# Kernel tuning notes

Hardware: AMD Instinct MI355X
Metric: run time of the kernel (lower is better)

## Reference

```python
import jax, jax.numpy as jnp
import numpy as np

BL = 5           # block_len
BS = BL * BL     # block_size = 25
NH = 8           # num_heads
MASK_ONES = 12   # first 12 window positions unmasked (causal raster mask)


def _rel_pos_index():
    coords = np.stack(np.meshgrid(np.arange(BL), np.arange(BL), indexing='ij')).reshape(2, -1)
    rel = coords[:, :, None] - coords[:, None, :]          # [2, 25, 25]
    idx = (rel[0] + BL - 1) * (2 * BL - 1) + (rel[1] + BL - 1)
    return idx                                              # [25, 25] int

_REL_IDX = _rel_pos_index()


def _layernorm(x, w, b, eps=1e-5):
    m = jnp.mean(x, axis=-1, keepdims=True)
    v = jnp.var(x, axis=-1, keepdims=True)
    return (x - m) * jax.lax.rsqrt(v + eps) * w + b


def setup_inputs() -> dict:
    key = jax.random.key(0)
    ks = jax.random.split(key, 16)
    B, C, H, W = 4, 64, 64, 64
    out_dim = 64
    hidden = int(C * 4.0)
    s = lambda k, shape, scale=0.02: jax.random.normal(k, shape, dtype=jnp.float32) * scale
    return {
        'x': jax.random.normal(ks[0], (B, C, H, W), dtype=jnp.float32),
        'norm1_w': jnp.ones((C,), jnp.float32), 'norm1_b': jnp.zeros((C,), jnp.float32),
        'qkv_w': s(ks[1], (3 * C, C)), 'qkv_b': s(ks[2], (3 * C,)),
        'rpb_table': s(ks[3], ((2 * BL - 1) * (2 * BL - 1), NH)),
        'norm2_w': jnp.ones((C,), jnp.float32), 'norm2_b': jnp.zeros((C,), jnp.float32),
        'fc1_w': s(ks[4], (hidden, C)), 'fc1_b': s(ks[5], (hidden,)),
        'fc2_w': s(ks[6], (C, hidden)), 'fc2_b': s(ks[7], (C,)),
        'proj_w': s(ks[8], (out_dim, C)), 'proj_b': s(ks[9], (out_dim,)),
    }


def reference(x, norm1_w, norm1_b, qkv_w, qkv_b, rpb_table,
              norm2_w, norm2_b, fc1_w, fc1_b, fc2_w, fc2_b, proj_w, proj_b):
    B, C, H, W = x.shape
    hd = C // NH
    scale = hd ** (-0.5)

    # F.unfold(kernel=5, pad=2): per-pixel 5x5 neighborhood, channel-major then (kh,kw)
    xp = jnp.pad(x, ((0, 0), (0, 0), (2, 2), (2, 2)))
    patches = jnp.stack([xp[:, :, i:i + H, j:j + W] for i in range(BL) for j in range(BL)], axis=2)  # [B,C,25,H,W]
    x_unfold = patches.reshape(B, C, BS, H * W).transpose(0, 3, 2, 1)  # [B,HW,25,C]

    mask = (jnp.arange(BS) < MASK_ONES).astype(x.dtype)[None, None, :, None]
    x_masked = x_unfold * mask

    out = _layernorm(x_masked, norm1_w, norm1_b)
    qkv = out @ qkv_w.T + qkv_b                                 # [B,HW,25,3C]
    qkv = qkv.reshape(B, H * W, BS, 3, NH, hd).transpose(3, 0, 1, 4, 2, 5)  # [3,B,HW,nh,25,hd]
    q, k, v = qkv[0] * scale, qkv[1], qkv[2]

    attn = jnp.einsum('bpnqd,bpnkd->bpnqk', q, k)               # [B,HW,nh,25,25]
    bias = rpb_table[_REL_IDX.reshape(-1)].reshape(BS, BS, NH).transpose(2, 0, 1)  # [nh,25,25]
    attn = jax.nn.softmax(attn + bias[None, None], axis=-1)

    o = jnp.einsum('bpnqk,bpnkd->bpnqd', attn, v)               # [B,HW,nh,25,hd]
    o = o.transpose(0, 1, 3, 2, 4).reshape(B, H * W, BS, C)
    o = o + x_masked
    out_sumed = jnp.sum(o, axis=2)                              # [B,HW,C]

    y = _layernorm(out_sumed, norm2_w, norm2_b)
    y = jax.nn.gelu(y @ fc1_w.T + fc1_b, approximate=False) @ fc2_w.T + fc2_b
    y = y + out_sumed
    y = y @ proj_w.T + proj_b                                   # [B,HW,out_dim]
    return y.reshape(B, H, W, -1).transpose(0, 3, 1, 2)
```

## Files before the change

### kernel.cpp

```cpp
#include <hip/hip_runtime.h>
#include <hip/hip_bf16.h>


typedef _Float16 h2f __attribute__((ext_vector_type(2)));

__device__ __forceinline__ float fdot2f(h2f a, h2f b, float c) {
#if defined(__has_builtin)
#if __has_builtin(__builtin_amdgcn_fdot2)
    return __builtin_amdgcn_fdot2(a, b, c, false);
#else
    return c + (float)a.x * (float)b.x + (float)a.y * (float)b.y;
#endif
#else
    return c + (float)a.x * (float)b.x + (float)a.y * (float)b.y;
#endif
}

__device__ __forceinline__ float frcp(float x) {
#if defined(__has_builtin)
#if __has_builtin(__builtin_amdgcn_rcpf)
    return __builtin_amdgcn_rcpf(x);
#else
    return 1.0f / x;
#endif
#else
    return 1.0f / x;
#endif
}

#define SC 0.35355339059327373f

__global__ __launch_bounds__(256) void k_qkv(
    const float* __restrict__ x, const float* __restrict__ n1w, const float* __restrict__ n1b,
    const float* __restrict__ qw, const float* __restrict__ qb, const float* __restrict__ rpb,
    float* __restrict__ qkv_all, float* __restrict__ qkvc,
    float* __restrict__ eb, float* __restrict__ ebs)
{
    const int t = threadIdx.x;
    if (blockIdx.x == 256) {
        if (t < 192) {
            float acc = qb[t];
            for (int c = 0; c < 64; ++c) acc += n1b[c] * qw[t * 64 + c];
            qkvc[t] = acc;
        }
        for (int i = t; i < 2400; i += 256) {
            int h = i / 300, r = i % 300, q = r / 12, k = r % 12;
            int idx = (q / 5 - k / 5 + 4) * 9 + (q % 5 - k % 5 + 4);
            eb[i] = __expf(rpb[idx * 8 + h]);
        }
        for (int i = t; i < 200; i += 256) {
            int h = i / 25, q = i % 25;
            float s = 0.f;
            for (int k = 12; k < 25; ++k) {
                int idx = (q / 5 - k / 5 + 4) * 9 + (q % 5 - k % 5 + 4);
                s += __expf(rpb[idx * 8 + h]);
            }
            ebs[i] = s;
        }
        return;
    }
    __shared__ float sw[12288];
    for (int i = t * 4; i < 12288; i += 1024)
        *(float4*)(sw + i) = *(const float4*)(qw + i);
    __syncthreads();
    const int lane = t & 63, g = t >> 6;
    const int p = blockIdx.x * 64 + lane;
    const int b = p >> 12, hw = p & 4095;
    const float* xp = x + b * 262144 + hw;
    float xr[64];
    float s = 0.f;
#pragma unroll
    for (int c = 0; c < 64; ++c) { float v = xp[c * 4096]; xr[c] = v; s += v; }
    float m = s * 0.015625f;
    float s2 = 0.f;
#pragma unroll
    for (int c = 0; c < 64; ++c) { float d = xr[c] - m; s2 += d * d; }
    float rstd = rsqrtf(s2 * 0.015625f + 1e-5f);
#pragma unroll
    for (int c = 0; c < 64; ++c) xr[c] = (xr[c] - m) * rstd * n1w[c] + n1b[c];
    float* orow = qkv_all + (size_t)p * 192;
    for (int i = 0; i < 48; ++i) {
        int o = g * 48 + i;
        const float* wr = sw + o * 64;
        float acc = qb[o];
#pragma unroll
        for (int c = 0; c < 64; ++c) acc += xr[c] * wr[c];
        orow[o] = acc;
    }
}

__global__ __launch_bounds__(256) void k_attn(
    const float* __restrict__ x, const float* __restrict__ qkv_all,
    const float* __restrict__ qkvc, const float* __restrict__ eb, const float* __restrict__ ebs,
    float* __restrict__ osT)
{
    __shared__ float sq[108 * 194];
    __shared__ float sx[108 * 66];
    __shared__ float seb[2400];
    __shared__ float sebs[200];
    __shared__ float sqc[192];
    const int t = threadIdx.x;
    const int p0 = blockIdx.x * 32;
    const int b = p0 >> 12;
    const int hw0 = p0 & 4095;
    const int hrow = hw0 >> 6, w0 = hw0 & 63;

    for (int i = t; i < 192; i += 256) sqc[i] = qkvc[i];
    for (int i = t; i < 2400; i += 256) seb[i] = eb[i];
    for (int i = t; i < 200; i += 256) sebs[i] = ebs[i];
    for (int idx = t; idx < 108 * 96; idx += 256) {
        int row = idx / 96, o2 = (idx - row * 96) * 2;
        int rr = row / 36, cc = row - rr * 36;
        int gr = hrow - 2 + rr, gc = w0 - 2 + cc;
        float2 v;
        if (gr >= 0 && gc >= 0 && gc < 64)
            v = *(const float2*)(qkv_all + (size_t)((b << 12) + (gr << 6) + gc) * 192 + o2);
        else
            v = make_float2(qkvc[o2], qkvc[o2 + 1]);
        *(float2*)(sq + row * 194 + o2) = v;
    }
    for (int idx = t; idx < 6912; idx += 256) {
        int r = idx / 2304, rem = idx - r * 2304, c = rem / 36, ww = rem - c * 36;
        int gr = hrow - 2 + r, gc = w0 - 2 + ww;
        float v = (gr >= 0 && gc >= 0 && gc < 64) ? x[b * 262144 + c * 4096 + (gr << 6) + gc] : 0.f;
        sx[(r * 36 + ww) * 66 + c] = v;
    }
    __syncthreads();

    const int pix = t & 31, h = t >> 5, hb = h * 8;

    float xs[8];
#pragma unroll
    for (int d = 0; d < 8; ++d) xs[d] = 0.f;
#pragma unroll
    for (int s = 0; s < 12; ++s) {
        const float* xr = sx + ((s / 5) * 36 + pix + (s % 5)) * 66 + hb;
#pragma unroll
        for (int d = 0; d < 8; ++d) xs[d] += xr[d];
    }
    float qch[8];
#pragma unroll
    for (int d = 0; d < 8; ++d) qch[d] = sqc[hb + d] * SC;
    float edc[12], ecc;
#pragma unroll
    for (int k = 0; k < 13; ++k) {
        const float* kp = (k < 12) ? (sq + ((k / 5) * 36 + pix + (k % 5)) * 194 + 64 + hb)
                                   : (sqc + 64 + hb);
        float dd = 0.f;
#pragma unroll
        for (int d = 0; d < 8; ++d) dd += qch[d] * kp[d];
        if (k < 12) edc[k] = __expf(dd); else ecc = __expf(dd);
    }
    float w[12], wc = 0.f;
#pragma unroll
    for (int k = 0; k < 12; ++k) w[k] = 0.f;

#pragma unroll
    for (int qc = 0; qc < 3; ++qc) {
        float qr[4][8];
#pragma unroll
        for (int qq = 0; qq < 4; ++qq) {
            const int s = qc * 4 + qq;
            const float* qp = sq + ((s / 5) * 36 + pix + (s % 5)) * 194 + hb;
#pragma unroll
            for (int d = 0; d < 8; ++d) qr[qq][d] = qp[d] * SC;
        }
        float er[4][13];
#pragma unroll
        for (int k = 0; k < 13; ++k) {
            float kr[8];
            const float* kp = (k < 12) ? (sq + ((k / 5) * 36 + pix + (k % 5)) * 194 + 64 + hb)
                                       : (sqc + 64 + hb);
#pragma unroll
            for (int d = 0; d < 8; ++d) kr[d] = kp[d];
#pragma unroll
            for (int qq = 0; qq < 4; ++qq) {
                float dd = 0.f;
#pragma unroll
                for (int d = 0; d < 8; ++d) dd += qr[qq][d] * kr[d];
                er[qq][k] = dd;
            }
        }
#pragma unroll
        for (int qq = 0; qq < 4; ++qq) {
            const int s = qc * 4 + qq;
            const float* ebr = seb + (h * 25 + s) * 12;
            float ebsv = sebs[h * 25 + s];
            float ec = __expf(er[qq][12]);
            float tt[12];
            float rs = ec * ebsv;
#pragma unroll
            for (int k = 0; k < 12; ++k) { float e = __expf(er[qq][k]) * ebr[k]; tt[k] = e; rs += e; }
            float inv = frcp(rs);
#pragma unroll
            for (int k = 0; k < 12; ++k) w[k] += tt[k] * inv;
            wc += ec * ebsv * inv;
        }
    }
#pragma unroll
    for (int q = 12; q < 25; ++q) {
        const float* ebr = seb + (h * 25 + q) * 12;
        float ebsv = sebs[h * 25 + q];
        float rs = ecc * ebsv;
        float tt[12];
#pragma unroll
        for (int k = 0; k < 12; ++k) { float e = edc[k] * ebr[k]; tt[k] = e; rs += e; }
        float inv = frcp(rs);
#pragma unroll
        for (int k = 0; k < 12; ++k) w[k] += tt[k] * inv;
        wc += ecc * ebsv * inv;
    }
    float out[8];
#pragma unroll
    for (int d = 0; d < 8; ++d) out[d] = wc * sqc[128 + hb + d];
#pragma unroll
    for (int k = 0; k < 12; ++k) {
        const float* vr = sq + ((k / 5) * 36 + pix + (k % 5)) * 194 + 128 + hb;
#pragma unroll
        for (int d = 0; d < 8; ++d) out[d] += w[k] * vr[d];
    }
    const int p = p0 + pix;
#pragma unroll
    for (int d = 0; d < 8; ++d) osT[(size_t)(hb + d) * 16384 + p] = out[d] + xs[d];
}

__global__ __launch_bounds__(512) void k_mlp(
    const float* __restrict__ osT, const float* __restrict__ n2w, const float* __restrict__ n2b,
    const float* __restrict__ w1, const float* __restrict__ b1,
    const float* __restrict__ w2, const float* __restrict__ b2,
    const float* __restrict__ pw, const float* __restrict__ pb,
    float* __restrict__ out)
{
    __shared__ _Float16 sW1[16384];
    __shared__ _Float16 sW2[16384];
    __shared__ float sP[4096];
    __shared__ _Float16 sH[64 * 258];
    __shared__ float sY[64 * 66];
    __shared__ float sb1[256], sb2[64], spb[64];
    const int t = threadIdx.x;
    for (int i = t; i < 16384; i += 512) sW1[i] = (_Float16)w1[i];
    for (int i = t; i < 16384; i += 512) sW2[i] = (_Float16)w2[i];
    for (int i = t; i < 4096; i += 512) sP[i] = pw[i];
    if (t < 256) sb1[t] = b1[t];
    if (t < 64) { sb2[t] = b2[t]; spb[t] = pb[t]; }
    __syncthreads();
    const int pix = t & 63, sl = t >> 6;
    const int p = blockIdx.x * 64 + pix;
    float a[64];
    float s = 0.f;
#pragma unroll
    for (int c = 0; c < 64; ++c) { float v = osT[(size_t)c * 16384 + p]; a[c] = v; s += v; }
    float m = s * 0.015625f;
    float s2 = 0.f;
#pragma unroll
    for (int c = 0; c < 64; ++c) { float d = a[c] - m; s2 += d * d; }
    float rstd = rsqrtf(s2 * 0.015625f + 1e-5f);
    h2f av[32];
#pragma unroll
    for (int c = 0; c < 32; ++c) {
        float e0 = (a[2 * c] - m) * rstd * n2w[2 * c] + n2b[2 * c];
        float e1 = (a[2 * c + 1] - m) * rstd * n2w[2 * c + 1] + n2b[2 * c + 1];
        h2f v; v.x = (_Float16)e0; v.y = (_Float16)e1;
        av[c] = v;
    }
    for (int i = 0; i < 32; ++i) {
        int j = sl * 32 + i;
        const h2f* wr = (const h2f*)(sW1 + j * 64);
        float acc = sb1[j];
#pragma unroll
        for (int cp = 0; cp < 32; ++cp) acc = fdot2f(av[cp], wr[cp], acc);
        float g = 0.5f * acc * (1.f + erff(acc * 0.70710678118654752f));
        sH[pix * 258 + j] = (_Float16)g;
    }
    __syncthreads();
#pragma unroll
    for (int mm = 0; mm < 8; ++mm) {
        int o = sl * 8 + mm;
        const h2f* wr = (const h2f*)(sW2 + o * 256);
        const h2f* hr = (const h2f*)(sH + pix * 258);
        float acc = sb2[o];
#pragma unroll 32
        for (int jp = 0; jp < 128; ++jp) acc = fdot2f(hr[jp], wr[jp], acc);
        float resid = osT[(size_t)o * 16384 + p];
        sY[pix * 66 + o] = acc + resid;
    }
    __syncthreads();
    const int bimg = p >> 12, hw = p & 4095, hh = hw >> 6, ww = hw & 63;
#pragma unroll
    for (int mm = 0; mm < 8; ++mm) {
        int o = sl * 8 + mm;
        const float* wr = sP + o * 64;
        const float* yr = sY + pix * 66;
        float acc = spb[o];
#pragma unroll
        for (int c = 0; c < 64; ++c) acc += yr[c] * wr[c];
        out[(size_t)(((bimg * 64 + o) * 64 + hh) * 64) + ww] = acc;
    }
}

extern "C" void kernel_launch(void* const* d_in, const int* in_sizes, int n_in,
                              void* d_out, int out_size, void* d_ws, size_t ws_size,
                              hipStream_t stream) {
    const float* x   = (const float*)d_in[0];
    const float* n1w = (const float*)d_in[1];
    const float* n1b = (const float*)d_in[2];
    const float* qw  = (const float*)d_in[3];
    const float* qb  = (const float*)d_in[4];
    const float* rpb = (const float*)d_in[5];
    const float* n2w = (const float*)d_in[6];
    const float* n2b = (const float*)d_in[7];
    const float* w1  = (const float*)d_in[8];
    const float* b1  = (const float*)d_in[9];
    const float* w2  = (const float*)d_in[10];
    const float* b2  = (const float*)d_in[11];
    const float* pw  = (const float*)d_in[12];
    const float* pb  = (const float*)d_in[13];
    float* out = (float*)d_out;

    float* ws = (float*)d_ws;
    float* qkv_all = ws;
    float* osT     = qkv_all + 16384 * 192;
    float* qkvc    = osT + 64 * 16384;
    float* eb      = qkvc + 192;
    float* ebs     = eb + 2400;

    hipLaunchKernelGGL(k_qkv, dim3(257), dim3(256), 0, stream,
                       x, n1w, n1b, qw, qb, rpb, qkv_all, qkvc, eb, ebs);
    hipLaunchKernelGGL(k_attn, dim3(512), dim3(256), 0, stream,
                       x, qkv_all, qkvc, eb, ebs, osT);
    hipLaunchKernelGGL(k_mlp, dim3(256), dim3(512), 0, stream,
                       osT, n2w, n2b, w1, b1, w2, b2, pw, pb, out);
}
```

Baseline: 224.0 us.

## Store QKV in fp16, split attention queries across halves, precompute fp16 MLP weights

The QKV projection now uses fp16 dot2 instructions and writes fp16 qkv, which halves the intermediate traffic. The masked x-window residual sum moves into extra blocks of the first kernel, and attention then accumulates into osT. Attention uses 512 threads with the query set split across two halves, reduced through shared memory, and K held in registers as fp16x8. The MLP kernel reads weights that were converted to fp16 once in global memory instead of converting them per block into LDS, and it now uses 32-pixel tiles. These changes lower precision and add a read-modify-write dependency on osT.

```diff
diff --git a/kernel.cpp b/kernel.cpp
--- a/kernel.cpp
+++ b/kernel.cpp
@@ -3,298 +3,329 @@
 
 
 typedef _Float16 h2f __attribute__((ext_vector_type(2)));
+typedef _Float16 h8  __attribute__((ext_vector_type(8)));
+union u8h { h8 v; h2f p[4]; };
 
 __device__ __forceinline__ float fdot2f(h2f a, h2f b, float c) {
 #if defined(__has_builtin)
 #if __has_builtin(__builtin_amdgcn_fdot2)
     return __builtin_amdgcn_fdot2(a, b, c, false);
 #else
-    return c + (float)a.x * (float)b.x + (float)a.y * (float)b.y;
+    return c + (float)a.x*(float)b.x + (float)a.y*(float)b.y;
 #endif
 #else
-    return c + (float)a.x * (float)b.x + (float)a.y * (float)b.y;
+    return c + (float)a.x*(float)b.x + (float)a.y*(float)b.y;
 #endif
 }
-
+__device__ __forceinline__ float dot8(u8h a, u8h b) {
+    float c = 0.f;
+    c = fdot2f(a.p[0], b.p[0], c);
+    c = fdot2f(a.p[1], b.p[1], c);
+    c = fdot2f(a.p[2], b.p[2], c);
+    c = fdot2f(a.p[3], b.p[3], c);
+    return c;
+}
 __device__ __forceinline__ float frcp(float x) {
 #if defined(__has_builtin)
 #if __has_builtin(__builtin_amdgcn_rcpf)
     return __builtin_amdgcn_rcpf(x);
 #else
-    return 1.0f / x;
+    return 1.0f/x;
 #endif
 #else
-    return 1.0f / x;
+    return 1.0f/x;
 #endif
 }
 
 #define SC 0.35355339059327373f
 
-__global__ __launch_bounds__(256) void k_qkv(
+__global__ __launch_bounds__(256, 4) void k_qkv(
     const float* __restrict__ x, const float* __restrict__ n1w, const float* __restrict__ n1b,
     const float* __restrict__ qw, const float* __restrict__ qb, const float* __restrict__ rpb,
-    float* __restrict__ qkv_all, float* __restrict__ qkvc,
-    float* __restrict__ eb, float* __restrict__ ebs)
+    const float* __restrict__ w1, const float* __restrict__ w2, const float* __restrict__ pw,
+    _Float16* __restrict__ qkv, _Float16* __restrict__ qkvc_h,
+    _Float16* __restrict__ ebh, float* __restrict__ ebs,
+    _Float16* __restrict__ w1h, _Float16* __restrict__ w2h, _Float16* __restrict__ pwh,
+    float* __restrict__ osT)
 {
     const int t = threadIdx.x;
-    if (blockIdx.x == 256) {
-        if (t < 192) {
-            float acc = qb[t];
-            for (int c = 0; c < 64; ++c) acc += n1b[c] * qw[t * 64 + c];
-            qkvc[t] = acc;
+    const int bid = blockIdx.x;
+    if (bid >= 512) {
+        if (bid == 768) {
+            if (t < 192) {
+                float acc = qb[t];
+                for (int c = 0; c < 64; ++c) acc += n1b[c]*qw[t*64 + c];
+                qkvc_h[t] = (_Float16)acc;
+            }
+            for (int i = t; i < 2400; i += 256) {
+                int h = i/300, r = i%300, q = r/12, k = r%12;
+                int idx = (q/5 - k/5 + 4)*9 + (q%5 - k%5 + 4);
+                ebh[i] = (_Float16)__expf(rpb[idx*8 + h]);
+            }
+            for (int i = t; i < 200; i += 256) {
+                int h = i/25, q = i%25; float s = 0.f;
+                for (int k = 12; k < 25; ++k) {
+                    int idx = (q/5 - k/5 + 4)*9 + (q%5 - k%5 + 4);
+                    s += __expf(rpb[idx*8 + h]);
+                }
+                ebs[i] = s;
+            }
+            for (int i = t; i < 16384; i += 256) w1h[i] = (_Float16)w1[i];
+            for (int i = t; i < 16384; i += 256) w2h[i] = (_Float16)w2[i];
+            for (int i = t; i < 4096;  i += 256) pwh[i] = (_Float16)pw[i];
+            return;
         }
-        for (int i = t; i < 2400; i += 256) {
-            int h = i / 300, r = i % 300, q = r / 12, k = r % 12;
-            int idx = (q / 5 - k / 5 + 4) * 9 + (q % 5 - k % 5 + 4);
-            eb[i] = __expf(rpb[idx * 8 + h]);
-        }
-        for (int i = t; i < 200; i += 256) {
-            int h = i / 25, q = i % 25;
+        for (int i = 0; i < 16; ++i) {
+            int idx = (bid - 512)*4096 + i*256 + t;
+            int c = idx >> 14, p = idx & 16383, b = p >> 12, hw = p & 4095;
+            int hh = hw >> 6, ww = hw & 63;
+            const float* pl = x + b*262144 + c*4096;
             float s = 0.f;
-            for (int k = 12; k < 25; ++k) {
-                int idx = (q / 5 - k / 5 + 4) * 9 + (q % 5 - k % 5 + 4);
-                s += __expf(rpb[idx * 8 + h]);
+            #pragma unroll
+            for (int dr = -2; dr <= 0; ++dr) {
+                int r = hh + dr; if (r < 0) continue;
+                int cmax = (dr == 0) ? -1 : 2;
+                #pragma unroll
+                for (int dc = -2; dc <= 2; ++dc) {
+                    if (dc > cmax) break;
+                    int w2c = ww + dc;
+                    if (w2c >= 0 && w2c < 64) s += pl[(r << 6) + w2c];
+                }
             }
-            ebs[i] = s;
+            osT[(size_t)c*16384 + p] = s;
         }
         return;
     }
-    __shared__ float sw[12288];
-    for (int i = t * 4; i < 12288; i += 1024)
-        *(float4*)(sw + i) = *(const float4*)(qw + i);
-    __syncthreads();
-    const int lane = t & 63, g = t >> 6;
-    const int p = blockIdx.x * 64 + lane;
-    const int b = p >> 12, hw = p & 4095;
-    const float* xp = x + b * 262144 + hw;
-    float xr[64];
-    float s = 0.f;
-#pragma unroll
-    for (int c = 0; c < 64; ++c) { float v = xp[c * 4096]; xr[c] = v; s += v; }
-    float m = s * 0.015625f;
-    float s2 = 0.f;
-#pragma unroll
-    for (int c = 0; c < 64; ++c) { float d = xr[c] - m; s2 += d * d; }
-    float rstd = rsqrtf(s2 * 0.015625f + 1e-5f);
-#pragma unroll
-    for (int c = 0; c < 64; ++c) xr[c] = (xr[c] - m) * rstd * n1w[c] + n1b[c];
-    float* orow = qkv_all + (size_t)p * 192;
-    for (int i = 0; i < 48; ++i) {
-        int o = g * 48 + i;
-        const float* wr = sw + o * 64;
+    __shared__ alignas(16) h2f sw[6144];
+    __shared__ float sX[2080];
+    __shared__ alignas(16) _Float16 sOut[6400];
+    for (int i = t; i < 6144; i += 256) {
+        float2 v = *(const float2*)(qw + i*2);
+        sw[i] = h2f{(_Float16)v.x, (_Float16)v.y};
+    }
+    const int p0 = bid*32;
+    const int b = p0 >> 12, hw0 = p0 & 4095;
+    for (int i = t; i < 2048; i += 256) {
+        int c = i >> 5, pp = i & 31;
+        sX[pp*65 + c] = x[b*262144 + c*4096 + hw0 + pp];
+    }
+    __syncthreads();
+    const int pix = t & 31, g = t >> 5;
+    float s = 0.f, s2 = 0.f;
+    #pragma unroll
+    for (int c = 0; c < 64; ++c) { float v = sX[pix*65 + c]; s += v; s2 += v*v; }
+    float m = s*0.015625f;
+    float rstd = rsqrtf(fmaxf(s2*0.015625f - m*m, 0.f) + 1e-5f);
+    h2f av[32];
+    #pragma unroll
+    for (int c = 0; c < 32; ++c) {
+        float e0 = (sX[pix*65 + 2*c]     - m)*rstd*n1w[2*c]     + n1b[2*c];
+        float e1 = (sX[pix*65 + 2*c + 1] - m)*rstd*n1w[2*c + 1] + n1b[2*c + 1];
+        av[c] = h2f{(_Float16)e0, (_Float16)e1};
+    }
+    for (int i = 0; i < 24; ++i) {
+        int o = g*24 + i;
+        const h2f* wr = sw + o*32;
         float acc = qb[o];
-#pragma unroll
-        for (int c = 0; c < 64; ++c) acc += xr[c] * wr[c];
-        orow[o] = acc;
-    }
-}
-
-__global__ __launch_bounds__(256) void k_attn(
-    const float* __restrict__ x, const float* __restrict__ qkv_all,
-    const float* __restrict__ qkvc, const float* __restrict__ eb, const float* __restrict__ ebs,
+        #pragma unroll
+        for (int cp = 0; cp < 32; ++cp) acc = fdot2f(av[cp], wr[cp], acc);
+        sOut[pix*200 + o] = (_Float16)acc;
+    }
+    __syncthreads();
+    for (int i = t; i < 768; i += 256) {
+        int pp = i/24, d4 = i%24;
+        ((float4*)qkv)[(size_t)p0*24 + i] = *(const float4*)(sOut + pp*200 + d4*8);
+    }
+}
+
+__global__ __launch_bounds__(512, 4) void k_attn(
+    const _Float16* __restrict__ qkv, const _Float16* __restrict__ qkvc_h,
+    const _Float16* __restrict__ ebh, const float* __restrict__ ebs,
     float* __restrict__ osT)
 {
-    __shared__ float sq[108 * 194];
-    __shared__ float sx[108 * 66];
-    __shared__ float seb[2400];
+    __shared__ alignas(16) _Float16 sq[21600];
+    __shared__ _Float16 seb[2400];
     __shared__ float sebs[200];
-    __shared__ float sqc[192];
+    __shared__ alignas(16) _Float16 sqc[192];
+    __shared__ float red[6656];
     const int t = threadIdx.x;
-    const int p0 = blockIdx.x * 32;
-    const int b = p0 >> 12;
-    const int hw0 = p0 & 4095;
-    const int hrow = hw0 >> 6, w0 = hw0 & 63;
-
-    for (int i = t; i < 192; i += 256) sqc[i] = qkvc[i];
-    for (int i = t; i < 2400; i += 256) seb[i] = eb[i];
-    for (int i = t; i < 200; i += 256) sebs[i] = ebs[i];
-    for (int idx = t; idx < 108 * 96; idx += 256) {
-        int row = idx / 96, o2 = (idx - row * 96) * 2;
-        int rr = row / 36, cc = row - rr * 36;
+    const int p0 = blockIdx.x*32;
+    const int b = p0 >> 12, hw0 = p0 & 4095, hrow = hw0 >> 6, w0 = hw0 & 63;
+
+    for (int i = t; i < 1200; i += 512) ((float*)seb)[i] = ((const float*)ebh)[i];
+    for (int i = t; i < 200; i += 512) sebs[i] = ebs[i];
+    if (t < 96) ((float*)sqc)[t] = ((const float*)qkvc_h)[t];
+    for (int i = t; i < 2592; i += 512) {
+        int row = i/24, d4 = i%24;
+        int rr = row/36, cc = row%36;
         int gr = hrow - 2 + rr, gc = w0 - 2 + cc;
-        float2 v;
+        float4 v;
         if (gr >= 0 && gc >= 0 && gc < 64)
-            v = *(const float2*)(qkv_all + (size_t)((b << 12) + (gr << 6) + gc) * 192 + o2);
+            v = ((const float4*)qkv)[(size_t)((b << 12) + (gr << 6) + gc)*24 + d4];
         else
-            v = make_float2(qkvc[o2], qkvc[o2 + 1]);
-        *(float2*)(sq + row * 194 + o2) = v;
-    }
-    for (int idx = t; idx < 6912; idx += 256) {
-        int r = idx / 2304, rem = idx - r * 2304, c = rem / 36, ww = rem - c * 36;
-        int gr = hrow - 2 + r, gc = w0 - 2 + ww;
-        float v = (gr >= 0 && gc >= 0 && gc < 64) ? x[b * 262144 + c * 4096 + (gr << 6) + gc] : 0.f;
-        sx[(r * 36 + ww) * 66 + c] = v;
-    }
-    __syncthreads();
-
-    const int pix = t & 31, h = t >> 5, hb = h * 8;
-
-    float xs[8];
-#pragma unroll
-    for (int d = 0; d < 8; ++d) xs[d] = 0.f;
-#pragma unroll
-    for (int s = 0; s < 12; ++s) {
-        const float* xr = sx + ((s / 5) * 36 + pix + (s % 5)) * 66 + hb;
-#pragma unroll
-        for (int d = 0; d < 8; ++d) xs[d] += xr[d];
-    }
-    float qch[8];
-#pragma unroll
-    for (int d = 0; d < 8; ++d) qch[d] = sqc[hb + d] * SC;
-    float edc[12], ecc;
-#pragma unroll
-    for (int k = 0; k < 13; ++k) {
-        const float* kp = (k < 12) ? (sq + ((k / 5) * 36 + pix + (k % 5)) * 194 + 64 + hb)
-                                   : (sqc + 64 + hb);
-        float dd = 0.f;
-#pragma unroll
-        for (int d = 0; d < 8; ++d) dd += qch[d] * kp[d];
-        if (k < 12) edc[k] = __expf(dd); else ecc = __expf(dd);
-    }
-    float w[12], wc = 0.f;
-#pragma unroll
-    for (int k = 0; k < 12; ++k) w[k] = 0.f;
-
-#pragma unroll
-    for (int qc = 0; qc < 3; ++qc) {
-        float qr[4][8];
-#pragma unroll
-        for (int qq = 0; qq < 4; ++qq) {
-            const int s = qc * 4 + qq;
-            const float* qp = sq + ((s / 5) * 36 + pix + (s % 5)) * 194 + hb;
-#pragma unroll
-            for (int d = 0; d < 8; ++d) qr[qq][d] = qp[d] * SC;
+            v = ((const float4*)qkvc_h)[d4];
+        *(float4*)(sq + row*200 + d4*8) = v;
+    }
+    __syncthreads();
+
+    const int pix = t & 31, h = (t >> 5) & 7, half = t >> 8, hb = h*8;
+    u8h kreg[12];
+    #pragma unroll
+    for (int k = 0; k < 12; ++k) {
+        int rw = (k/5)*36 + pix + (k%5);
+        kreg[k].v = *(const h8*)(sq + rw*200 + 64 + hb);
+    }
+    u8h kc; kc.v = *(const h8*)(sqc + 64 + hb);
+
+    float w[13];
+    #pragma unroll
+    for (int k = 0; k < 13; ++k) w[k] = 0.f;
+
+    const int qlo = half ? 9 : 0, qhi = half ? 12 : 9;
+    for (int sIdx = qlo; sIdx < qhi; ++sIdx) {
+        int rw = (sIdx/5)*36 + pix + (sIdx%5);
+        u8h qu; qu.v = *(const h8*)(sq + rw*200 + hb);
+        const _Float16* ebr = seb + (h*25 + sIdx)*12;
+        float rs = __expf(dot8(qu, kc)*SC) * sebs[h*25 + sIdx];
+        float wcq = rs;
+        float tt[12];
+        #pragma unroll
+        for (int k = 0; k < 12; ++k) {
+            float e = __expf(dot8(qu, kreg[k])*SC) * (float)ebr[k];
+            tt[k] = e; rs += e;
         }
-        float er[4][13];
-#pragma unroll
-        for (int k = 0; k < 13; ++k) {
-            float kr[8];
-            const float* kp = (k < 12) ? (sq + ((k / 5) * 36 + pix + (k % 5)) * 194 + 64 + hb)
-                                       : (sqc + 64 + hb);
-#pragma unroll
-            for (int d = 0; d < 8; ++d) kr[d] = kp[d];
-#pragma unroll
-            for (int qq = 0; qq < 4; ++qq) {
-                float dd = 0.f;
-#pragma unroll
-                for (int d = 0; d < 8; ++d) dd += qr[qq][d] * kr[d];
-                er[qq][k] = dd;
-            }
+        float inv = frcp(rs);
+        #pragma unroll
+        for (int k = 0; k < 12; ++k) w[k] += tt[k]*inv;
+        w[12] += wcq*inv;
+    }
+    if (half) {
+        u8h qcu; qcu.v = *(const h8*)(sqc + hb);
+        float edc[12];
+        #pragma unroll
+        for (int k = 0; k < 12; ++k) edc[k] = __expf(dot8(qcu, kreg[k])*SC);
+        float ecc = __expf(dot8(qcu, kc)*SC);
+        for (int q = 12; q < 25; ++q) {
+            const _Float16* ebr = seb + (h*25 + q)*12;
+            float rs = ecc * sebs[h*25 + q];
+            float wcq = rs;
+            float tt[12];
+            #pragma unroll
+            for (int k = 0; k < 12; ++k) { float e = edc[k]*(float)ebr[k]; tt[k] = e; rs += e; }
+            float inv = frcp(rs);
+            #pragma unroll
+            for (int k = 0; k < 12; ++k) w[k] += tt[k]*inv;
+            w[12] += wcq*inv;
         }
-#pragma unroll
-        for (int qq = 0; qq < 4; ++qq) {
-            const int s = qc * 4 + qq;
-            const float* ebr = seb + (h * 25 + s) * 12;
-            float ebsv = sebs[h * 25 + s];
-            float ec = __expf(er[qq][12]);
-            float tt[12];
-            float rs = ec * ebsv;
-#pragma unroll
-            for (int k = 0; k < 12; ++k) { float e = __expf(er[qq][k]) * ebr[k]; tt[k] = e; rs += e; }
-            float inv = frcp(rs);
-#pragma unroll
-            for (int k = 0; k < 12; ++k) w[k] += tt[k] * inv;
-            wc += ec * ebsv * inv;
-        }
-    }
-#pragma unroll
-    for (int q = 12; q < 25; ++q) {
-        const float* ebr = seb + (h * 25 + q) * 12;
-        float ebsv = sebs[h * 25 + q];
-        float rs = ecc * ebsv;
-        float tt[12];
-#pragma unroll
-        for (int k = 0; k < 12; ++k) { float e = edc[k] * ebr[k]; tt[k] = e; rs += e; }
-        float inv = frcp(rs);
-#pragma unroll
-        for (int k = 0; k < 12; ++k) w[k] += tt[k] * inv;
-        wc += ecc * ebsv * inv;
-    }
-    float out[8];
-#pragma unroll
-    for (int d = 0; d < 8; ++d) out[d] = wc * sqc[128 + hb + d];
-#pragma unroll
+    }
+    const int ph = (h << 5) + pix;
+    {
+        float* my = red + (ph*2 + half)*13;
+        #pragma unroll
+        for (int k = 0; k < 13; ++k) my[k] = w[k];
+    }
+    __syncthreads();
+    {
+        const float* ot = red + (ph*2 + (half ^ 1))*13;
+        #pragma unroll
+        for (int k = 0; k < 13; ++k) w[k] += ot[k];
+    }
+    const int d0 = half*4;
+    float out0, out1, out2, out3;
+    {
+        const h2f* vcp = (const h2f*)(sqc + 128 + hb + d0);
+        h2f v0 = vcp[0], v1 = vcp[1];
+        out0 = w[12]*(float)v0.x; out1 = w[12]*(float)v0.y;
+        out2 = w[12]*(float)v1.x; out3 = w[12]*(float)v1.y;
+    }
+    #pragma unroll
     for (int k = 0; k < 12; ++k) {
-        const float* vr = sq + ((k / 5) * 36 + pix + (k % 5)) * 194 + 128 + hb;
-#pragma unroll
-        for (int d = 0; d < 8; ++d) out[d] += w[k] * vr[d];
+        int rw = (k/5)*36 + pix + (k%5);
+        const h2f* vp = (const h2f*)(sq + rw*200 + 128 + hb + d0);
+        h2f v0 = vp[0], v1 = vp[1];
+        float wk = w[k];
+        out0 += wk*(float)v0.x; out1 += wk*(float)v0.y;
+        out2 += wk*(float)v1.x; out3 += wk*(float)v1.y;
     }
     const int p = p0 + pix;
-#pragma unroll
-    for (int d = 0; d < 8; ++d) osT[(size_t)(hb + d) * 16384 + p] = out[d] + xs[d];
-}
-
-__global__ __launch_bounds__(512) void k_mlp(
+    float* op = osT + (size_t)(hb + d0)*16384 + p;
+    op[0]       += out0;
+    op[16384]   += out1;
+    op[32768]   += out2;
+    op[49152]   += out3;
+}
+
+__global__ __launch_bounds__(512, 4) void k_mlp(
     const float* __restrict__ osT, const float* __restrict__ n2w, const float* __restrict__ n2b,
-    const float* __restrict__ w1, const float* __restrict__ b1,
-    const float* __restrict__ w2, const float* __restrict__ b2,
-    const float* __restrict__ pw, const float* __restrict__ pb,
+    const float* __restrict__ b1, const float* __restrict__ b2, const float* __restrict__ pb,
+    const _Float16* __restrict__ w1h, const _Float16* __restrict__ w2h, const _Float16* __restrict__ pwh,
     float* __restrict__ out)
 {
-    __shared__ _Float16 sW1[16384];
-    __shared__ _Float16 sW2[16384];
-    __shared__ float sP[4096];
-    __shared__ _Float16 sH[64 * 258];
-    __shared__ float sY[64 * 66];
-    __shared__ float sb1[256], sb2[64], spb[64];
+    __shared__ float sA[2112];
+    __shared__ h2f sAv[1088];
+    __shared__ alignas(16) _Float16 sH[8448];
+    __shared__ alignas(16) _Float16 sY[2304];
+    __shared__ float sb1[256], sb2[64], spb[64], sM[32], sR[32], sN[128];
     const int t = threadIdx.x;
-    for (int i = t; i < 16384; i += 512) sW1[i] = (_Float16)w1[i];
-    for (int i = t; i < 16384; i += 512) sW2[i] = (_Float16)w2[i];
-    for (int i = t; i < 4096; i += 512) sP[i] = pw[i];
+    const int p0 = blockIdx.x*32;
+    for (int i = t; i < 2048; i += 512) {
+        int c = i >> 5, pp = i & 31;
+        sA[pp*66 + c] = osT[(size_t)c*16384 + p0 + pp];
+    }
     if (t < 256) sb1[t] = b1[t];
-    if (t < 64) { sb2[t] = b2[t]; spb[t] = pb[t]; }
-    __syncthreads();
-    const int pix = t & 63, sl = t >> 6;
-    const int p = blockIdx.x * 64 + pix;
-    float a[64];
-    float s = 0.f;
-#pragma unroll
-    for (int c = 0; c < 64; ++c) { float v = osT[(size_t)c * 16384 + p]; a[c] = v; s += v; }
-    float m = s * 0.015625f;
-    float s2 = 0.f;
-#pragma unroll
-    for (int c = 0; c < 64; ++c) { float d = a[c] - m; s2 += d * d; }
-    float rstd = rsqrtf(s2 * 0.015625f + 1e-5f);
-    h2f av[32];
-#pragma unroll
-    for (int c = 0; c < 32; ++c) {
-        float e0 = (a[2 * c] - m) * rstd * n2w[2 * c] + n2b[2 * c];
-        float e1 = (a[2 * c + 1] - m) * rstd * n2w[2 * c + 1] + n2b[2 * c + 1];
-        h2f v; v.x = (_Float16)e0; v.y = (_Float16)e1;
-        av[c] = v;
-    }
-    for (int i = 0; i < 32; ++i) {
-        int j = sl * 32 + i;
-        const h2f* wr = (const h2f*)(sW1 + j * 64);
+    else if (t < 320) sb2[t - 256] = b2[t - 256];
+    else if (t < 384) spb[t - 320] = pb[t - 320];
+    else if (t < 448) sN[t - 384] = n2w[t - 384];
+    else sN[64 + (t - 448)] = n2b[t - 448];
+    __syncthreads();
+    if (t < 32) {
+        float s = 0.f, s2 = 0.f;
+        for (int c = 0; c < 64; ++c) { float v = sA[t*66 + c]; s += v; s2 += v*v; }
+        float m = s*0.015625f;
+        sM[t] = m; sR[t] = rsqrtf(fmaxf(s2*0.015625f - m*m, 0.f) + 1e-5f);
+    }
+    __syncthreads();
+    for (int i = t; i < 1024; i += 512) {
+        int pp = i >> 5, pr = i & 31;
+        float m = sM[pp], r = sR[pp];
+        float e0 = (sA[pp*66 + 2*pr]     - m)*r*sN[2*pr]     + sN[64 + 2*pr];
+        float e1 = (sA[pp*66 + 2*pr + 1] - m)*r*sN[2*pr + 1] + sN[64 + 2*pr + 1];
+        sAv[pp*34 + pr] = h2f{(_Float16)e0, (_Float16)e1};
+    }
+    __syncthreads();
+    const int pix = t & 31, sl = t >> 5;
+    const int p = p0 + pix;
+    const h2f* avr = sAv + pix*34;
+    for (int i = 0; i < 16; ++i) {
+        int j = sl*16 + i;
+        const h2f* wr = (const h2f*)(w1h + j*64);
         float acc = sb1[j];
-#pragma unroll
-        for (int cp = 0; cp < 32; ++cp) acc = fdot2f(av[cp], wr[cp], acc);
-        float g = 0.5f * acc * (1.f + erff(acc * 0.70710678118654752f));
-        sH[pix * 258 + j] = (_Float16)g;
-    }
-    __syncthreads();
-#pragma unroll
-    for (int mm = 0; mm < 8; ++mm) {
-        int o = sl * 8 + mm;
-        const h2f* wr = (const h2f*)(sW2 + o * 256);
-        const h2f* hr = (const h2f*)(sH + pix * 258);
+        #pragma unroll
+        for (int cp = 0; cp < 32; ++cp) acc = fdot2f(avr[cp], wr[cp], acc);
+        float g = 0.5f*acc*(1.f + erff(acc*0.70710678118654752f));
+        sH[pix*264 + j] = (_Float16)g;
+    }
+    __syncthreads();
+    const h2f* hr = (const h2f*)(sH + pix*264);
+    for (int mm = 0; mm < 4; ++mm) {
+        int o = sl*4 + mm;
+        const h2f* wr = (const h2f*)(w2h + o*256);
         float acc = sb2[o];
-#pragma unroll 32
+        #pragma unroll 32
         for (int jp = 0; jp < 128; ++jp) acc = fdot2f(hr[jp], wr[jp], acc);
-        float resid = osT[(size_t)o * 16384 + p];
-        sY[pix * 66 + o] = acc + resid;
+        float y = acc + osT[(size_t)o*16384 + p];
+        sY[pix*72 + o] = (_Float16)y;
     }
     __syncthreads();
     const int bimg = p >> 12, hw = p & 4095, hh = hw >> 6, ww = hw & 63;
-#pragma unroll
-    for (int mm = 0; mm < 8; ++mm) {
-        int o = sl * 8 + mm;
-        const float* wr = sP + o * 64;
-        const float* yr = sY + pix * 66;
+    const h2f* yr = (const h2f*)(sY + pix*72);
+    for (int mm = 0; mm < 4; ++mm) {
+        int o = sl*4 + mm;
+        const h2f* wr = (const h2f*)(pwh + o*64);
         float acc = spb[o];
-#pragma unroll
-        for (int c = 0; c < 64; ++c) acc += yr[c] * wr[c];
-        out[(size_t)(((bimg * 64 + o) * 64 + hh) * 64) + ww] = acc;
+        #pragma unroll
+        for (int c = 0; c < 32; ++c) acc = fdot2f(yr[c], wr[c], acc);
+        out[(size_t)(((bimg*64 + o)*64 + hh)*64) + ww] = acc;
     }
 }
 
@@ -318,16 +349,20 @@
     float* out = (float*)d_out;
 
     float* ws = (float*)d_ws;
-    float* qkv_all = ws;
-    float* osT     = qkv_all + 16384 * 192;
-    float* qkvc    = osT + 64 * 16384;
-    float* eb      = qkvc + 192;
-    float* ebs     = eb + 2400;
-
-    hipLaunchKernelGGL(k_qkv, dim3(257), dim3(256), 0, stream,
-                       x, n1w, n1b, qw, qb, rpb, qkv_all, qkvc, eb, ebs);
-    hipLaunchKernelGGL(k_attn, dim3(512), dim3(256), 0, stream,
-                       x, qkv_all, qkvc, eb, ebs, osT);
-    hipLaunchKernelGGL(k_mlp, dim3(256), dim3(512), 0, stream,
-                       osT, n2w, n2b, w1, b1, w2, b2, pw, pb, out);
-}
+    _Float16* qkv    = (_Float16*)ws;
+    float*    osT    = ws + 1572864;
+    _Float16* qkvc_h = (_Float16*)(ws + 2621440);
+    _Float16* ebh    = (_Float16*)(ws + 2621536);
+    float*    ebsp   = ws + 2622736;
+    _Float16* w1h    = (_Float16*)(ws + 2622936);
+    _Float16* w2h    = (_Float16*)(ws + 2631128);
+    _Float16* pwh    = (_Float16*)(ws + 2639320);
+
+    hipLaunchKernelGGL(k_qkv, dim3(769), dim3(256), 0, stream,
+                       x, n1w, n1b, qw, qb, rpb, w1, w2, pw,
+                       qkv, qkvc_h, ebh, ebsp, w1h, w2h, pwh, osT);
+    hipLaunchKernelGGL(k_attn, dim3(512), dim3(512), 0, stream,
+                       qkv, qkvc_h, ebh, ebsp, osT);
+    hipLaunchKernelGGL(k_mlp, dim3(512), dim3(512), 0, stream,
+                       osT, n2w, n2b, b1, b2, pb, w1h, w2h, pwh, out);
+}
```

Result: faster. 190.3 us (-15.0%).
